# Optimization experiments

Measured on AMD Instinct MI355X. Metric: run time of the kernel, lower is better.

The kernel has to match this reference:

```python
import jax, jax.numpy as jnp
import numpy as np
import math

D_MODEL = 1024
NUM_HEADS = 16
D_FF = 4096
EPS = 1e-5
BATCH = 2
SEQ = 2048


def _trunc_normal(key, shape, std):
    # truncated normal on [-3std, 3std], matching nn.init.trunc_normal_
    return std * jax.random.truncated_normal(key, -3.0, 3.0, shape, dtype=jnp.float32)


def setup_inputs() -> dict:
    key = jax.random.key(0)
    ks = jax.random.split(key, 8)
    x = jax.random.normal(ks[0], (BATCH, SEQ, D_MODEL), dtype=jnp.float32)
    std_dd = math.sqrt(2.0 / (D_MODEL + D_MODEL))
    std_up = math.sqrt(2.0 / (D_MODEL + D_FF))
    # Linear stores W as [out_features, in_features]; forward does x @ W.T
    W_q = _trunc_normal(ks[1], (D_MODEL, D_MODEL), std_dd)
    W_k = _trunc_normal(ks[2], (D_MODEL, D_MODEL), std_dd)
    W_v = _trunc_normal(ks[3], (D_MODEL, D_MODEL), std_dd)
    W_o = _trunc_normal(ks[4], (D_MODEL, D_MODEL), std_dd)
    W1 = _trunc_normal(ks[5], (D_FF, D_MODEL), std_up)
    W2 = _trunc_normal(ks[6], (D_MODEL, D_FF), std_up)
    ln1_w = jnp.ones((D_MODEL,), jnp.float32)
    ln1_b = jnp.zeros((D_MODEL,), jnp.float32)
    ln2_w = jnp.ones((D_MODEL,), jnp.float32)
    ln2_b = jnp.zeros((D_MODEL,), jnp.float32)
    return {"x": x, "W_q": W_q, "W_k": W_k, "W_v": W_v, "W_o": W_o,
            "W1": W1, "W2": W2,
            "ln1_w": ln1_w, "ln1_b": ln1_b, "ln2_w": ln2_w, "ln2_b": ln2_b}


def _layernorm(x, w, b):
    xf = x.astype(jnp.float32)
    mean = xf.mean(axis=-1, keepdims=True)
    var = jnp.mean((xf - mean) ** 2, axis=-1, keepdims=True)
    xn = (xf - mean) / jnp.sqrt(var + EPS)
    return (xn * w.astype(jnp.float32) + b.astype(jnp.float32)).astype(x.dtype)


def _attention(x, W_q, W_k, W_v, W_o):
    B, S, D = x.shape
    H, dk = NUM_HEADS, D // NUM_HEADS
    Q = (x @ W_q.T).reshape(B, S, H, dk).transpose(0, 2, 1, 3)  # [B,H,S,dk]
    K = (x @ W_k.T).reshape(B, S, H, dk).transpose(0, 2, 1, 3)
    V = (x @ W_v.T).reshape(B, S, H, dk).transpose(0, 2, 1, 3)
    scores = jnp.einsum('bhqd,bhkd->bhqk', Q, K) / math.sqrt(dk)
    causal = jnp.tril(jnp.ones((S, S), dtype=bool))
    scores = jnp.where(causal, scores, -jnp.inf)
    attn = jax.nn.softmax(scores, axis=-1)
    out = jnp.einsum('bhqk,bhkd->bhqd', attn, V)  # [B,H,S,dk]
    out = out.transpose(0, 2, 1, 3).reshape(B, S, D)
    return out @ W_o.T


def _ffn(x, W1, W2):
    h = x @ W1.T
    h = h * (h > 0)  # ReLU
    return h @ W2.T


def reference(x, W_q, W_k, W_v, W_o, W1, W2, ln1_w, ln1_b, ln2_w, ln2_b):
    x = x + _attention(_layernorm(x, ln1_w, ln1_b), W_q, W_k, W_v, W_o)
    x = x + _ffn(_layernorm(x, ln2_w, ln2_b), W1, W2)
    return x
```

## Files before the change

kernel.cpp:

```cpp
#include <hip/hip_runtime.h>
#include <stdint.h>

typedef unsigned short u16;
typedef unsigned int u32;
typedef __bf16 bf16x8 __attribute__((ext_vector_type(8)));
typedef float f32x4 __attribute__((ext_vector_type(4)));
typedef unsigned short u16x8 __attribute__((ext_vector_type(8)));
typedef unsigned short u16x4 __attribute__((ext_vector_type(4)));
typedef u16x8 u16x8_a __attribute__((may_alias));
typedef u16x4 u16x4_a __attribute__((may_alias));

#define DEV static __device__ __forceinline__

DEV u16 f2bf(float f) {
  unsigned u = __builtin_bit_cast(unsigned, f);
  u += 0x7fffu + ((u >> 16) & 1u);
  return (u16)(u >> 16);
}
DEV bf16x8 ld8(const u16* p) {
  u16x8 v = *(const u16x8_a*)p;
  return __builtin_bit_cast(bf16x8, v);
}
DEV f32x4 vmax4(f32x4 a, f32x4 b) {
  f32x4 r;
  r[0] = fmaxf(a[0], b[0]); r[1] = fmaxf(a[1], b[1]);
  r[2] = fmaxf(a[2], b[2]); r[3] = fmaxf(a[3], b[3]);
  return r;
}
DEV void swz_block(int& bx, int& by) {
  const int gx = gridDim.x;
  const int nwg = gx * gridDim.y;
  int lin = by * gx + bx;
  const int q = nwg >> 3, r = nwg & 7, x = lin & 7, p = lin >> 3;
  lin = (x < r ? x * (q + 1) : r * (q + 1) + (x - r) * q) + p;
  bx = lin % gx; by = lin / gx;
}

#define GL_LDS16(gp, lp)                                                        \
  __builtin_amdgcn_global_load_lds(                                             \
      (const __attribute__((address_space(1))) void*)(gp),                      \
      (__attribute__((address_space(3))) void*)(lp), 16, 0, 0)

#define VMW8 asm volatile("s_waitcnt vmcnt(8)" ::: "memory")
#define VMW4 asm volatile("s_waitcnt vmcnt(4)" ::: "memory")
#define VMW2 asm volatile("s_waitcnt vmcnt(2)" ::: "memory")
#define VMW0 asm volatile("s_waitcnt vmcnt(0)" ::: "memory")
#define BAR  __builtin_amdgcn_s_barrier()

__global__ __launch_bounds__(256) void cvt_k(const float* __restrict__ s,
                                             u16* __restrict__ d, int n4) {
  int i = blockIdx.x * 256 + threadIdx.x;
  if (i < n4) {
    float4 v = ((const float4*)s)[i];
    u16x4 o;
    o[0] = f2bf(v.x); o[1] = f2bf(v.y); o[2] = f2bf(v.z); o[3] = f2bf(v.w);
    *(u16x4_a*)(d + (size_t)i * 4) = o;
  }
}

__global__ __launch_bounds__(256) void ln_k(const float* __restrict__ x,
                                            const float* __restrict__ w,
                                            const float* __restrict__ b,
                                            u16* __restrict__ o) {
  const int row = blockIdx.x, t = threadIdx.x;
  const float4 v = ((const float4*)(x + (size_t)row * 1024))[t];
  float s = v.x + v.y + v.z + v.w;
  float q = v.x * v.x + v.y * v.y + v.z * v.z + v.w * v.w;
#pragma unroll
  for (int m = 1; m < 64; m <<= 1) { s += __shfl_xor(s, m); q += __shfl_xor(q, m); }
  __shared__ float ss[4], qq[4];
  if ((t & 63) == 0) { ss[t >> 6] = s; qq[t >> 6] = q; }
  __syncthreads();
  s = ss[0] + ss[1] + ss[2] + ss[3];
  q = qq[0] + qq[1] + qq[2] + qq[3];
  const float mean = s * (1.f / 1024.f);
  const float var = q * (1.f / 1024.f) - mean * mean;
  const float rstd = rsqrtf(var + 1e-5f);
  const float4 wv = ((const float4*)w)[t];
  const float4 bv = ((const float4*)b)[t];
  u16x4 ov;
  ov[0] = f2bf((v.x - mean) * rstd * wv.x + bv.x);
  ov[1] = f2bf((v.y - mean) * rstd * wv.y + bv.y);
  ov[2] = f2bf((v.z - mean) * rstd * wv.z + bv.z);
  ov[3] = f2bf((v.w - mean) * rstd * wv.w + bv.w);
  *(u16x4_a*)(o + (size_t)row * 1024 + t * 4) = ov;
}

__global__ __launch_bounds__(256) void vtr_k(const u16* __restrict__ qkvV,
                                             u16* __restrict__ vt) {
  __shared__ u16 T[64][65];
  const int st = blockIdx.x, bh = blockIdx.y;
  const int b = bh >> 4, h = bh & 15;
  const int t = threadIdx.x;
  const u16* src = qkvV + ((size_t)(b * 2048 + st * 64)) * 3072 + h * 64;
  const int r = t >> 2, c0 = (t & 3) * 16;
  u16x8 a0 = *(const u16x8_a*)(src + (size_t)r * 3072 + c0);
  u16x8 a1 = *(const u16x8_a*)(src + (size_t)r * 3072 + c0 + 8);
#pragma unroll
  for (int e = 0; e < 8; ++e) { T[r][c0 + e] = a0[e]; T[r][c0 + 8 + e] = a1[e]; }
  __syncthreads();
  const int d = t >> 2, s0 = (t & 3) * 16;
  u16x8 o0, o1;
#pragma unroll
  for (int e = 0; e < 8; ++e) { o0[e] = T[s0 + e][d]; o1[e] = T[s0 + 8 + e][d]; }
  u16* dst = vt + ((size_t)bh * 64 + d) * 2048 + (size_t)st * 64 + s0;
  *(u16x8_a*)dst = o0;
  *(u16x8_a*)(dst + 8) = o1;
}

DEV void stage_op(const u16* __restrict__ G, int K, int kk, u16* lds, int set,
                  int isB, int w, int l) {
#pragma unroll
  for (int i = 0; i < 2; ++i) {
    const int c = i * 8 + w;
    int rb;
    if (!isB) { const int lr = c * 8; rb = (lr < 64 ? lr : lr + 64) + set * 64; }
    else      { rb = (c >> 2) * 64 + set * 32 + (c & 3) * 8; }
    const int row = rb + (l >> 3);
    const int c8 = (l & 7) ^ (row & 7);
    GL_LDS16(G + (size_t)row * K + kk + c8 * 8, lds + rb * 64);
  }
}
DEV void rdA(const u16* as, int wr, int mh, int l15, int l4, bf16x8 af[4][2]) {
#pragma unroll
  for (int f = 0; f < 4; ++f) {
    const int row = wr * 128 + mh * 64 + f * 16 + l15;
#pragma unroll
    for (int ks = 0; ks < 2; ++ks) {
      const int c8 = (ks * 4 + l4) ^ (row & 7);
      af[f][ks] = ld8(as + row * 64 + c8 * 8);
    }
  }
}
DEV void rdB(const u16* bs, int wc, int nh, int l15, int l4, bf16x8 bf_[2][2]) {
#pragma unroll
  for (int g = 0; g < 2; ++g) {
    const int row = wc * 64 + nh * 32 + g * 16 + l15;
#pragma unroll
    for (int ks = 0; ks < 2; ++ks) {
      const int c8 = (ks * 4 + l4) ^ (row & 7);
      bf_[g][ks] = ld8(bs + row * 64 + c8 * 8);
    }
  }
}

#define MFMA16(mh, nh)                                                          \
  __builtin_amdgcn_s_setprio(1);                                                \
  _Pragma("unroll")                                                             \
  for (int f = 0; f < 4; ++f) {                                                 \
    _Pragma("unroll")                                                           \
    for (int g = 0; g < 2; ++g) {                                               \
      f32x4& a_ = acc[(mh) * 4 + f][(nh) * 2 + g];                              \
      a_ = __builtin_amdgcn_mfma_f32_16x16x32_bf16(af[f][0], bfr[g][0], a_, 0, 0, 0); \
      a_ = __builtin_amdgcn_mfma_f32_16x16x32_bf16(af[f][1], bfr[g][1], a_, 0, 0, 0); \
    }                                                                           \
  }                                                                             \
  __builtin_amdgcn_s_setprio(0);

template <int EPI>
__global__ __launch_bounds__(512, 2) void gemm8(const u16* __restrict__ A,
                                                const u16* __restrict__ Bw,
                                                u16* __restrict__ Cp,
                                                int M, int N, int K, int qcols) {
  __shared__ __align__(16) u16 As[2][256 * 64];
  __shared__ __align__(16) u16 Bs[2][256 * 64];
  const int t = threadIdx.x, w = t >> 6, l = t & 63;
  const int l15 = l & 15, l4 = l >> 4;
  const int wr = w >> 2, wc = w & 3;
  int bx = blockIdx.x, by = blockIdx.y;
  swz_block(bx, by);
  const int bm0 = by * 256, bn0 = bx * 256;
  const u16* Ab = A + (size_t)bm0 * K;
  const u16* Bb = Bw + (size_t)bn0 * K;

  f32x4 acc[8][4] = {};
  stage_op(Ab, K, 0, As[0], 0, 0, w, l);
  stage_op(Bb, K, 0, Bs[0], 0, 1, w, l);
  stage_op(Bb, K, 0, Bs[0], 1, 1, w, l);
  stage_op(Ab, K, 0, As[0], 1, 0, w, l);
  VMW4;
  BAR;

  const int nk = K >> 6;
  int cur = 0;
  bf16x8 af[4][2], bfr[2][2];
  for (int kt = 0; kt < nk; ++kt) {
    const int kn = (kt + 1) << 6;
    const bool more = (kt + 1 < nk);
    u16* An = As[cur ^ 1];
    u16* Bn = Bs[cur ^ 1];
    rdA(As[cur], wr, 0, l15, l4, af);
    rdB(Bs[cur], wc, 0, l15, l4, bfr);
    if (more) stage_op(Ab, K, kn, An, 0, 0, w, l);
    BAR;
    MFMA16(0, 0)
    if (more) { VMW4; } else { VMW2; }
    BAR;
    rdB(Bs[cur], wc, 1, l15, l4, bfr);
    if (more) stage_op(Bb, K, kn, Bn, 0, 1, w, l);
    BAR;
    MFMA16(0, 1)
    if (more) { VMW4; } else { VMW0; }
    BAR;
    rdA(As[cur], wr, 1, l15, l4, af);
    if (more) stage_op(Bb, K, kn, Bn, 1, 1, w, l);
    BAR;
    MFMA16(1, 1)
    BAR;
    rdB(Bs[cur], wc, 0, l15, l4, bfr);
    if (more) stage_op(Ab, K, kn, An, 1, 0, w, l);
    BAR;
    MFMA16(1, 0)
    if (more) { VMW4; }
    BAR;
    cur ^= 1;
  }

#pragma unroll
  for (int m = 0; m < 8; ++m) {
    const int row0 = bm0 + wr * 128 + m * 16 + l4 * 4;
#pragma unroll
    for (int n = 0; n < 4; ++n) {
      const int col = bn0 + wc * 64 + n * 16 + l15;
      const float qs = (col < qcols) ? 0.125f : 1.f;
#pragma unroll
      for (int r = 0; r < 4; ++r) {
        float v = acc[m][n][r] * qs;
        if constexpr (EPI == 1) v = v > 0.f ? v : 0.f;
        Cp[(size_t)(row0 + r) * N + col] = f2bf(v);
      }
    }
  }
}

__global__ __launch_bounds__(512, 1) void gemm128(const u16* __restrict__ A,
                                                  const u16* __restrict__ Bw,
                                                  float* __restrict__ C,
                                                  const float* __restrict__ res,
                                                  int M, int N, int K) {
  __shared__ __align__(16) u16 As[3][128 * 64];
  __shared__ __align__(16) u16 Bs[3][128 * 64];
  const int t = threadIdx.x, w = t >> 6, l = t & 63;
  const int l15 = l & 15, l4 = l >> 4;
  const int wr = w >> 2, wc = w & 3;
  int bx = blockIdx.x, by = blockIdx.y;
  swz_block(bx, by);
  const int bm0 = by * 128, bn0 = bx * 128;
  const u16* Ab = A + (size_t)bm0 * K;
  const u16* Bb = Bw + (size_t)bn0 * K;

  auto stg = [&](const u16* __restrict__ G, u16* lds, int kk) {
#pragma unroll
    for (int i = 0; i < 2; ++i) {
      const int c = i * 8 + w;
      const int row = c * 8 + (l >> 3);
      const int c8 = (l & 7) ^ (row & 7);
      GL_LDS16(G + (size_t)row * K + kk + c8 * 8, lds + c * 512);
    }
  };

  f32x4 acc[4][2] = {};
  stg(Ab, As[0], 0);  stg(Bb, Bs[0], 0);
  stg(Ab, As[1], 64); stg(Bb, Bs[1], 64);
  const int nk = K >> 6;
  for (int kt = 0; kt < nk; ++kt) {
    const int cur = kt % 3;
    if (kt + 2 < nk) {
      const int nxt = (kt + 2) % 3;
      const int kk = (kt + 2) << 6;
      stg(Ab, As[nxt], kk);
      stg(Bb, Bs[nxt], kk);
    }
    const int rem = nk - 1 - kt;
    if (rem >= 2) { VMW8; } else if (rem == 1) { VMW4; } else { VMW0; }
    BAR;
    bf16x8 af[4][2], bfr[2][2];
#pragma unroll
    for (int f = 0; f < 4; ++f) {
      const int row = wr * 64 + f * 16 + l15;
#pragma unroll
      for (int ks = 0; ks < 2; ++ks)
        af[f][ks] = ld8(&As[cur][row * 64 + (((ks * 4 + l4) ^ (row & 7)) * 8)]);
    }
#pragma unroll
    for (int g = 0; g < 2; ++g) {
      const int row = wc * 32 + g * 16 + l15;
#pragma unroll
      for (int ks = 0; ks < 2; ++ks)
        bfr[g][ks] = ld8(&Bs[cur][row * 64 + (((ks * 4 + l4) ^ (row & 7)) * 8)]);
    }
    __builtin_amdgcn_s_setprio(1);
#pragma unroll
    for (int f = 0; f < 4; ++f)
#pragma unroll
      for (int g = 0; g < 2; ++g) {
        acc[f][g] = __builtin_amdgcn_mfma_f32_16x16x32_bf16(af[f][0], bfr[g][0], acc[f][g], 0, 0, 0);
        acc[f][g] = __builtin_amdgcn_mfma_f32_16x16x32_bf16(af[f][1], bfr[g][1], acc[f][g], 0, 0, 0);
      }
    __builtin_amdgcn_s_setprio(0);
    BAR;
  }

#pragma unroll
  for (int f = 0; f < 4; ++f) {
    const int row0 = bm0 + wr * 64 + f * 16 + l4 * 4;
#pragma unroll
    for (int g = 0; g < 2; ++g) {
      const int col = bn0 + wc * 32 + g * 16 + l15;
#pragma unroll
      for (int r = 0; r < 4; ++r) {
        const size_t idx = (size_t)(row0 + r) * N + col;
        C[idx] = res[idx] + acc[f][g][r];
      }
    }
  }
}

__global__ __launch_bounds__(256) void attn_k(const u16* __restrict__ Qm,
                                              const u16* __restrict__ Km,
                                              const u16* __restrict__ vt,
                                              u16* __restrict__ Om) {
  const int S = 2048, D = 1024, ldq = 3072;
  int p = blockIdx.x, bh = blockIdx.y;
  swz_block(p, bh);
  const int bb = bh >> 4, h = bh & 15;
  const int t = threadIdx.x, w = t >> 6, l = t & 63, l15 = l & 15, l4 = l >> 4;
  const float NEGINF = -__builtin_inff();

  __shared__ __align__(16) u16 Ksm[2][64 * 64];
  __shared__ __align__(16) u16 Vsm[2][64 * 64];
  __shared__ __align__(16) u32 Psm[4][16 * 32];

  const u16* Qb = Qm + (size_t)bb * S * ldq + h * 64;
  const u16* Kb = Km + (size_t)bb * S * ldq + h * 64;
  const u16* Vtb = vt + (size_t)bh * 64 * 2048;

  auto stageKV = [&](int j, int buf) {
    const int k0 = j * 64;
#pragma unroll
    for (int i = 0; i < 2; ++i) {
      const int s = t + i * 256;
      const int row = s >> 3;
      const int colE = ((s & 7) ^ (row & 7)) * 8;
      GL_LDS16(Kb + (size_t)(k0 + row) * ldq + colE, &Ksm[buf][(s >> 6) * 512]);
      GL_LDS16(Vtb + (size_t)row * 2048 + k0 + colE, &Vsm[buf][(s >> 6) * 512]);
    }
  };

  u32* Pw = &Psm[w][0];
  const u16* Pu = (const u16*)Pw;
  const int h7 = l15 & 7;

  for (int half = 0; half < 2; ++half) {
    const int bx = half ? (31 - p) : p;
    const int q0 = bx * 64;
    __syncthreads();
    stageKV(0, 0);

    bf16x8 qf[2];
    const int qq = q0 + w * 16 + l15;
#pragma unroll
    for (int c = 0; c < 2; ++c) qf[c] = ld8(Qb + (size_t)qq * ldq + c * 32 + l4 * 8);

    f32x4 accT[4] = {};
    float mrow = NEGINF, lrow = 0.f;
    int cur = 0;

    for (int j = 0; j <= bx; ++j) {
      __syncthreads();
      if (j < bx) stageKV(j + 1, cur ^ 1);

      f32x4 sv[4] = {};
      __builtin_amdgcn_s_setprio(1);
#pragma unroll
      for (int c = 0; c < 2; ++c) {
#pragma unroll
        for (int nf = 0; nf < 4; ++nf) {
          const int row = nf * 16 + l15;
          bf16x8 kf = ld8(&Ksm[cur][row * 64 + ((c * 32 + l4 * 8) ^ ((row & 7) * 8))]);
          sv[nf] = __builtin_amdgcn_mfma_f32_16x16x32_bf16(kf, qf[c], sv[nf], 0, 0, 0);
        }
      }
      __builtin_amdgcn_s_setprio(0);

      if (j == bx) {
        const int k0 = j * 64;
#pragma unroll
        for (int nf = 0; nf < 4; ++nf) {
          const int kb = k0 + nf * 16 + l4 * 4;
#pragma unroll
          for (int r = 0; r < 4; ++r)
            if (kb + r > qq) sv[nf][r] = NEGINF;
        }
      }

      f32x4 m4 = vmax4(vmax4(sv[0], sv[1]), vmax4(sv[2], sv[3]));
      float mt = fmaxf(fmaxf(m4[0], m4[1]), fmaxf(m4[2], m4[3]));
      mt = fmaxf(mt, __shfl_xor(mt, 16));
      mt = fmaxf(mt, __shfl_xor(mt, 32));
      const bool skip = __all(mt - mrow <= 8.f);
      const float mnew = skip ? mrow : fmaxf(mrow, mt);
      if (!skip) {
        const float sf = __expf(mrow - mnew);
        lrow *= sf;
#pragma unroll
        for (int nf = 0; nf < 4; ++nf) accT[nf] *= sf;
        mrow = mnew;
      }
#pragma unroll
      for (int nf = 0; nf < 4; ++nf)
#pragma unroll
        for (int r = 0; r < 4; ++r) sv[nf][r] = __expf(sv[nf][r] - mnew);
      f32x4 s4 = (sv[0] + sv[1]) + (sv[2] + sv[3]);
      float ps = (s4[0] + s4[1]) + (s4[2] + s4[3]);
      ps += __shfl_xor(ps, 16);
      ps += __shfl_xor(ps, 32);
      lrow += ps;

#pragma unroll
      for (int nf = 0; nf < 4; ++nf) {
        u32 lo, hi;
        asm("v_cvt_pk_bf16_f32 %0, %1, %2" : "=v"(lo) : "v"(sv[nf][0]), "v"(sv[nf][1]));
        asm("v_cvt_pk_bf16_f32 %0, %1, %2" : "=v"(hi) : "v"(sv[nf][2]), "v"(sv[nf][3]));
        const int kw4 = (nf * 2 + (l4 >> 1)) ^ h7;
        const int base = l15 * 32 + kw4 * 4 + (l4 & 1) * 2;
        Pw[base] = lo;
        Pw[base + 1] = hi;
      }

      __builtin_amdgcn_s_setprio(1);
#pragma unroll
      for (int c = 0; c < 2; ++c) {
        bf16x8 pf = ld8(Pu + l15 * 64 + ((c * 4 + l4) ^ h7) * 8);
#pragma unroll
        for (int nf = 0; nf < 4; ++nf) {
          const int row = nf * 16 + l15;
          bf16x8 vf = ld8(&Vsm[cur][row * 64 + ((c * 32 + l4 * 8) ^ ((row & 7) * 8))]);
          accT[nf] = __builtin_amdgcn_mfma_f32_16x16x32_bf16(vf, pf, accT[nf], 0, 0, 0);
        }
      }
      __builtin_amdgcn_s_setprio(0);
      cur ^= 1;
    }

    const float inv = 1.f / lrow;
    u16* orow = Om + ((size_t)bb * S + qq) * D + h * 64;
#pragma unroll
    for (int nf = 0; nf < 4; ++nf) {
      u16x4 ov;
#pragma unroll
      for (int r = 0; r < 4; ++r) ov[r] = f2bf(accT[nf][r] * inv);
      *(u16x4_a*)(orow + nf * 16 + l4 * 4) = ov;
    }
  }
}

extern "C" void kernel_launch(void* const* d_in, const int* in_sizes, int n_in,
                              void* d_out, int out_size, void* d_ws, size_t ws_size,
                              hipStream_t stream) {
  (void)in_sizes; (void)n_in; (void)out_size; (void)ws_size;
  const float* x    = (const float*)d_in[0];
  const float* W_q  = (const float*)d_in[1];
  const float* W_k  = (const float*)d_in[2];
  const float* W_v  = (const float*)d_in[3];
  const float* W_o  = (const float*)d_in[4];
  const float* W1   = (const float*)d_in[5];
  const float* W2   = (const float*)d_in[6];
  const float* ln1w = (const float*)d_in[7];
  const float* ln1b = (const float*)d_in[8];
  const float* ln2w = (const float*)d_in[9];
  const float* ln2b = (const float*)d_in[10];

  const size_t MB = 1ull << 20;
  char* W = (char*)d_ws;
  u16* wqkv  = (u16*)(W + 0);
  u16* wo    = (u16*)(W + 6 * MB);
  u16* w1b   = (u16*)(W + 8 * MB);
  u16* w2b   = (u16*)(W + 16 * MB);
  u16* xn1   = (u16*)(W + 24 * MB);
  u16* qkv   = (u16*)(W + 32 * MB);
  u16* attnb = (u16*)(W + 56 * MB);
  u16* vt    = (u16*)(W + 64 * MB);
  u16* xn2   = (u16*)(W + 64 * MB);
  u16* hbuf  = (u16*)(W + 24 * MB);
  float* x2  = (float*)d_out;

  auto cvt = [&](const float* s, u16* d, int n) {
    int n4 = n >> 2;
    cvt_k<<<dim3((n4 + 255) / 256), dim3(256), 0, stream>>>(s, d, n4);
  };
  cvt(W_q, wqkv, 1 << 20);
  cvt(W_k, wqkv + (1 << 20), 1 << 20);
  cvt(W_v, wqkv + (2 << 20), 1 << 20);
  cvt(W_o, wo, 1 << 20);
  cvt(W1, w1b, 4 << 20);
  cvt(W2, w2b, 4 << 20);

  ln_k<<<dim3(4096), dim3(256), 0, stream>>>(x, ln1w, ln1b, xn1);
  gemm8<0><<<dim3(12, 16), dim3(512), 0, stream>>>(xn1, wqkv, qkv, 4096, 3072, 1024, 1024);
  vtr_k<<<dim3(32, 32), dim3(256), 0, stream>>>(qkv + 2048, vt);
  attn_k<<<dim3(16, 32), dim3(256), 0, stream>>>(qkv, qkv + 1024, vt, attnb);
  gemm128<<<dim3(8, 32), dim3(512), 0, stream>>>(attnb, wo, x2, x, 4096, 1024, 1024);
  ln_k<<<dim3(4096), dim3(256), 0, stream>>>(x2, ln2w, ln2b, xn2);
  gemm8<1><<<dim3(16, 16), dim3(512), 0, stream>>>(xn2, w1b, hbuf, 4096, 4096, 1024, 0);
  gemm128<<<dim3(8, 32), dim3(512), 0, stream>>>(hbuf, w2b, x2, x2, 4096, 1024, 4096);
}
```

Before: 246.0 us.

## Batch weight casts, fold log2e into Q scale, retile output GEMMs to 64x128

The six weight-conversion launches become one 2D-grid kernel, which removes launch overhead. The Q scale now includes log2(e), so attention can use exp2f directly and the rescale threshold is adjusted to match. The N=1024 output GEMMs change from 128x128 tiles with 512 threads and triple buffering to 64x128 tiles with 256 threads, two blocks per CU and double buffering. That doubles the grid to 512 blocks for better CU fill, at the cost of less operand reuse and a shallower prefetch pipeline.

```diff
diff --git a/kernel.cpp b/kernel.cpp
--- a/kernel.cpp
+++ b/kernel.cpp
@@ -41,20 +41,24 @@
       (const __attribute__((address_space(1))) void*)(gp),                      \
       (__attribute__((address_space(3))) void*)(lp), 16, 0, 0)
 
-#define VMW8 asm volatile("s_waitcnt vmcnt(8)" ::: "memory")
 #define VMW4 asm volatile("s_waitcnt vmcnt(4)" ::: "memory")
 #define VMW2 asm volatile("s_waitcnt vmcnt(2)" ::: "memory")
 #define VMW0 asm volatile("s_waitcnt vmcnt(0)" ::: "memory")
 #define BAR  __builtin_amdgcn_s_barrier()
 
-__global__ __launch_bounds__(256) void cvt_k(const float* __restrict__ s,
-                                             u16* __restrict__ d, int n4) {
-  int i = blockIdx.x * 256 + threadIdx.x;
-  if (i < n4) {
-    float4 v = ((const float4*)s)[i];
+struct Cvt6 {
+  const float* s[6];
+  u16* d[6];
+  int n4[6];
+};
+__global__ __launch_bounds__(256) void cvt6_k(Cvt6 c) {
+  const int yi = blockIdx.y;
+  const int i = blockIdx.x * 256 + threadIdx.x;
+  if (i < c.n4[yi]) {
+    float4 v = ((const float4*)c.s[yi])[i];
     u16x4 o;
     o[0] = f2bf(v.x); o[1] = f2bf(v.y); o[2] = f2bf(v.z); o[3] = f2bf(v.w);
-    *(u16x4_a*)(d + (size_t)i * 4) = o;
+    *(u16x4_a*)(c.d[yi] + (size_t)i * 4) = o;
   }
 }
 
@@ -222,7 +226,7 @@
 #pragma unroll
     for (int n = 0; n < 4; ++n) {
       const int col = bn0 + wc * 64 + n * 16 + l15;
-      const float qs = (col < qcols) ? 0.125f : 1.f;
+      const float qs = (col < qcols) ? 0.18033688f : 1.f;
 #pragma unroll
       for (int r = 0; r < 4; ++r) {
         float v = acc[m][n][r] * qs;
@@ -233,84 +237,86 @@
   }
 }
 
-__global__ __launch_bounds__(512, 1) void gemm128(const u16* __restrict__ A,
-                                                  const u16* __restrict__ Bw,
-                                                  float* __restrict__ C,
-                                                  const float* __restrict__ res,
-                                                  int M, int N, int K) {
-  __shared__ __align__(16) u16 As[3][128 * 64];
-  __shared__ __align__(16) u16 Bs[3][128 * 64];
+__global__ __launch_bounds__(256, 2) void gemm64(const u16* __restrict__ A,
+                                                 const u16* __restrict__ Bw,
+                                                 float* __restrict__ C,
+                                                 const float* __restrict__ res,
+                                                 int M, int N, int K) {
+  __shared__ __align__(16) u16 As[2][64 * 64];
+  __shared__ __align__(16) u16 Bs[2][128 * 64];
   const int t = threadIdx.x, w = t >> 6, l = t & 63;
   const int l15 = l & 15, l4 = l >> 4;
-  const int wr = w >> 2, wc = w & 3;
+  const int wr = w >> 1, wc = w & 1;
   int bx = blockIdx.x, by = blockIdx.y;
   swz_block(bx, by);
-  const int bm0 = by * 128, bn0 = bx * 128;
+  const int bm0 = by * 64, bn0 = bx * 128;
   const u16* Ab = A + (size_t)bm0 * K;
   const u16* Bb = Bw + (size_t)bn0 * K;
 
-  auto stg = [&](const u16* __restrict__ G, u16* lds, int kk) {
+  auto stgA = [&](int buf, int kk) {
 #pragma unroll
     for (int i = 0; i < 2; ++i) {
-      const int c = i * 8 + w;
-      const int row = c * 8 + (l >> 3);
+      const int s = t + i * 256;
+      const int row = s >> 3;
       const int c8 = (l & 7) ^ (row & 7);
-      GL_LDS16(G + (size_t)row * K + kk + c8 * 8, lds + c * 512);
+      GL_LDS16(Ab + (size_t)row * K + kk + c8 * 8, &As[buf][(s >> 6) * 512]);
     }
   };
-
-  f32x4 acc[4][2] = {};
-  stg(Ab, As[0], 0);  stg(Bb, Bs[0], 0);
-  stg(Ab, As[1], 64); stg(Bb, Bs[1], 64);
+  auto stgB = [&](int buf, int kk) {
+#pragma unroll
+    for (int i = 0; i < 4; ++i) {
+      const int s = t + i * 256;
+      const int row = s >> 3;
+      const int c8 = (l & 7) ^ (row & 7);
+      GL_LDS16(Bb + (size_t)row * K + kk + c8 * 8, &Bs[buf][(s >> 6) * 512]);
+    }
+  };
+
+  f32x4 acc[2][4] = {};
+  stgA(0, 0); stgB(0, 0);
   const int nk = K >> 6;
+  int cur = 0;
   for (int kt = 0; kt < nk; ++kt) {
-    const int cur = kt % 3;
-    if (kt + 2 < nk) {
-      const int nxt = (kt + 2) % 3;
-      const int kk = (kt + 2) << 6;
-      stg(Ab, As[nxt], kk);
-      stg(Bb, Bs[nxt], kk);
-    }
-    const int rem = nk - 1 - kt;
-    if (rem >= 2) { VMW8; } else if (rem == 1) { VMW4; } else { VMW0; }
-    BAR;
-    bf16x8 af[4][2], bfr[2][2];
-#pragma unroll
-    for (int f = 0; f < 4; ++f) {
-      const int row = wr * 64 + f * 16 + l15;
+    __syncthreads();
+    if (kt + 1 < nk) { stgA(cur ^ 1, (kt + 1) << 6); stgB(cur ^ 1, (kt + 1) << 6); }
+    bf16x8 af[2][2], bfr[4][2];
+#pragma unroll
+    for (int f = 0; f < 2; ++f) {
+      const int row = wr * 32 + f * 16 + l15;
 #pragma unroll
       for (int ks = 0; ks < 2; ++ks)
         af[f][ks] = ld8(&As[cur][row * 64 + (((ks * 4 + l4) ^ (row & 7)) * 8)]);
     }
 #pragma unroll
-    for (int g = 0; g < 2; ++g) {
-      const int row = wc * 32 + g * 16 + l15;
+    for (int n = 0; n < 4; ++n) {
+      const int row = wc * 64 + n * 16 + l15;
 #pragma unroll
       for (int ks = 0; ks < 2; ++ks)
-        bfr[g][ks] = ld8(&Bs[cur][row * 64 + (((ks * 4 + l4) ^ (row & 7)) * 8)]);
+        bfr[n][ks] = ld8(&Bs[cur][row * 64 + (((ks * 4 + l4) ^ (row & 7)) * 8)]);
     }
     __builtin_amdgcn_s_setprio(1);
 #pragma unroll
-    for (int f = 0; f < 4; ++f)
-#pragma unroll
-      for (int g = 0; g < 2; ++g) {
-        acc[f][g] = __builtin_amdgcn_mfma_f32_16x16x32_bf16(af[f][0], bfr[g][0], acc[f][g], 0, 0, 0);
-        acc[f][g] = __builtin_amdgcn_mfma_f32_16x16x32_bf16(af[f][1], bfr[g][1], acc[f][g], 0, 0, 0);
+    for (int f = 0; f < 2; ++f)
+#pragma unroll
+      for (int n = 0; n < 4; ++n) {
+        acc[f][n] = __builtin_amdgcn_mfma_f32_16x16x32_bf16(af[f][0], bfr[n][0], acc[f][n], 0, 0, 0);
+        acc[f][n] = __builtin_amdgcn_mfma_f32_16x16x32_bf16(af[f][1], bfr[n][1], acc[f][n], 0, 0, 0);
       }
     __builtin_amdgcn_s_setprio(0);
-    BAR;
-  }
-
-#pragma unroll
-  for (int f = 0; f < 4; ++f) {
-    const int row0 = bm0 + wr * 64 + f * 16 + l4 * 4;
-#pragma unroll
-    for (int g = 0; g < 2; ++g) {
-      const int col = bn0 + wc * 32 + g * 16 + l15;
+    __syncthreads();
+    cur ^= 1;
+  }
+
+#pragma unroll
+  for (int f = 0; f < 2; ++f) {
+    const int row0 = bm0 + wr * 32 + f * 16 + l4 * 4;
+#pragma unroll
+    for (int n = 0; n < 4; ++n) {
+      const int col = bn0 + wc * 64 + n * 16 + l15;
 #pragma unroll
       for (int r = 0; r < 4; ++r) {
         const size_t idx = (size_t)(row0 + r) * N + col;
-        C[idx] = res[idx] + acc[f][g][r];
+        C[idx] = res[idx] + acc[f][n][r];
       }
     }
   }
@@ -398,10 +404,10 @@
       float mt = fmaxf(fmaxf(m4[0], m4[1]), fmaxf(m4[2], m4[3]));
       mt = fmaxf(mt, __shfl_xor(mt, 16));
       mt = fmaxf(mt, __shfl_xor(mt, 32));
-      const bool skip = __all(mt - mrow <= 8.f);
+      const bool skip = __all(mt - mrow <= 11.54f);
       const float mnew = skip ? mrow : fmaxf(mrow, mt);
       if (!skip) {
-        const float sf = __expf(mrow - mnew);
+        const float sf = exp2f(mrow - mnew);
         lrow *= sf;
 #pragma unroll
         for (int nf = 0; nf < 4; ++nf) accT[nf] *= sf;
@@ -410,7 +416,7 @@
 #pragma unroll
       for (int nf = 0; nf < 4; ++nf)
 #pragma unroll
-        for (int r = 0; r < 4; ++r) sv[nf][r] = __expf(sv[nf][r] - mnew);
+        for (int r = 0; r < 4; ++r) sv[nf][r] = exp2f(sv[nf][r] - mnew);
       f32x4 s4 = (sv[0] + sv[1]) + (sv[2] + sv[3]);
       float ps = (s4[0] + s4[1]) + (s4[2] + s4[3]);
       ps += __shfl_xor(ps, 16);
@@ -485,23 +491,21 @@
   u16* hbuf  = (u16*)(W + 24 * MB);
   float* x2  = (float*)d_out;
 
-  auto cvt = [&](const float* s, u16* d, int n) {
-    int n4 = n >> 2;
-    cvt_k<<<dim3((n4 + 255) / 256), dim3(256), 0, stream>>>(s, d, n4);
-  };
-  cvt(W_q, wqkv, 1 << 20);
-  cvt(W_k, wqkv + (1 << 20), 1 << 20);
-  cvt(W_v, wqkv + (2 << 20), 1 << 20);
-  cvt(W_o, wo, 1 << 20);
-  cvt(W1, w1b, 4 << 20);
-  cvt(W2, w2b, 4 << 20);
+  Cvt6 c;
+  c.s[0] = W_q; c.d[0] = wqkv;              c.n4[0] = 1 << 18;
+  c.s[1] = W_k; c.d[1] = wqkv + (1 << 20);  c.n4[1] = 1 << 18;
+  c.s[2] = W_v; c.d[2] = wqkv + (2 << 20);  c.n4[2] = 1 << 18;
+  c.s[3] = W_o; c.d[3] = wo;                c.n4[3] = 1 << 18;
+  c.s[4] = W1;  c.d[4] = w1b;               c.n4[4] = 1 << 20;
+  c.s[5] = W2;  c.d[5] = w2b;               c.n4[5] = 1 << 20;
+  cvt6_k<<<dim3(4096, 6), dim3(256), 0, stream>>>(c);
 
   ln_k<<<dim3(4096), dim3(256), 0, stream>>>(x, ln1w, ln1b, xn1);
   gemm8<0><<<dim3(12, 16), dim3(512), 0, stream>>>(xn1, wqkv, qkv, 4096, 3072, 1024, 1024);
   vtr_k<<<dim3(32, 32), dim3(256), 0, stream>>>(qkv + 2048, vt);
   attn_k<<<dim3(16, 32), dim3(256), 0, stream>>>(qkv, qkv + 1024, vt, attnb);
-  gemm128<<<dim3(8, 32), dim3(512), 0, stream>>>(attnb, wo, x2, x, 4096, 1024, 1024);
+  gemm64<<<dim3(8, 64), dim3(256), 0, stream>>>(attnb, wo, x2, x, 4096, 1024, 1024);
   ln_k<<<dim3(4096), dim3(256), 0, stream>>>(x2, ln2w, ln2b, xn2);
   gemm8<1><<<dim3(16, 16), dim3(512), 0, stream>>>(xn2, w1b, hbuf, 4096, 4096, 1024, 0);
-  gemm128<<<dim3(8, 32), dim3(512), 0, stream>>>(hbuf, w2b, x2, x2, 4096, 1024, 4096);
-}
+  gemm64<<<dim3(8, 64), dim3(256), 0, stream>>>(hbuf, w2b, x2, x2, 4096, 1024, 4096);
+}
```

New measurement: 231.4 us. 1.06x faster.
